# Performance work log

Hardware: AMD Instinct MI355X
Metric: run time of the kernel (lower is better)

The kernel has to match this reference:

```python
import jax, jax.numpy as jnp
import numpy as np
import math


def setup_inputs() -> dict:
    key = jax.random.key(0)
    ks = jax.random.split(key, 10)
    B, N, C, heads = 16, 1024, 256, 8
    nW = 4
    ANGLE_BINS = 5
    inner = C  # dim_head*heads == dim
    return {
        "x": jax.random.normal(ks[0], (B, N, C), jnp.float32),
        "mask": jax.random.normal(ks[1], (nW, N, N), jnp.float32),
        "affine_matrix": jax.random.normal(ks[2], (B, 2, 3), jnp.float32),
        "Wq": jax.random.normal(ks[3], (C, inner), jnp.float32) * (C ** -0.5),
        "bq": jnp.zeros((inner,), jnp.float32),
        "Wkv": jax.random.normal(ks[4], (C, 2 * inner), jnp.float32) * (C ** -0.5),
        "bkv": jnp.zeros((2 * inner,), jnp.float32),
        "Wp": jax.random.normal(ks[5], (C, C), jnp.float32) * (C ** -0.5),
        "bp": jnp.zeros((C,), jnp.float32),
        "angle_table": jnp.ones((ANGLE_BINS, heads), jnp.float32),
        "H": 32,
        "W": 32,
    }


def reference(x, mask, affine_matrix, Wq, bq, Wkv, bkv, Wp, bp, angle_table, H, W):
    B, N, C = x.shape
    heads = angle_table.shape[1]
    hd = C // heads
    scale = hd ** -0.5

    # qkv projections (torch Linear -> x @ W + b with W stored as (in, out))
    q = (x @ Wq + bq).reshape(B, N, heads, hd).transpose(0, 2, 1, 3)      # (B,h,N,d)
    kv = (x @ Wkv + bkv).reshape(B, N, 2, heads, hd).transpose(2, 0, 3, 1, 4)
    k, v = kv[0], kv[1]                                                    # (B,h,N,d)

    attn = jnp.einsum('bhqd,bhkd->bhqk', q * scale, k)                     # (B,h,N,N)

    # angle bias: per-query multiplicative bias in (1,2)
    grid_y, grid_x = jnp.meshgrid(jnp.arange(H), jnp.arange(W), indexing='ij')
    coords = jnp.stack([grid_x.reshape(-1), grid_y.reshape(-1)], -1).astype(jnp.float32)  # (N,2)
    center = jnp.array([W / 2.0, H / 2.0], jnp.float32)
    ego = jnp.einsum('bij,j->bi', affine_matrix[:, :2, :2], center) + affine_matrix[:, :2, 2]  # (B,2)
    rel = coords[None, :, :] - ego[:, None, :]                             # (B,N,2)
    ang = jnp.arctan2(rel[..., 1], rel[..., 0])
    bins = (((ang + math.pi) / (2.0 * math.pi)) * (angle_table.shape[0] - 1)).astype(jnp.int32)
    bias = 1.0 + jax.nn.sigmoid(angle_table[bins])                         # (B,N,h)
    attn = attn * bias.transpose(0, 2, 1)[..., None]                       # broadcast over keys

    # additive window mask then softmax
    nW = mask.shape[0]
    attn = attn.reshape(B // nW, nW, heads, N, N) + mask[None, :, None]
    attn = jax.nn.softmax(attn.reshape(B, heads, N, N), axis=-1)

    out = jnp.einsum('bhqk,bhkd->bhqd', attn, v).transpose(0, 2, 1, 3).reshape(B, N, C)
    return out @ Wp + bp
```

## Files before the change

kernel.cpp:

```cpp
#include <hip/hip_runtime.h>
#include <hip/hip_bf16.h>
#include <math.h>

#define BB 16
#define NTOK 1024
#define CDIM 256
#define HEADS 8
#define HD 32
#define LOG2E 1.4426950408889634f
#define PSHIFT 18.0f

typedef __attribute__((ext_vector_type(8))) _Float16 half8;
typedef __attribute__((ext_vector_type(4))) _Float16 half4v;
typedef __attribute__((ext_vector_type(8))) unsigned short u16x8;
typedef __attribute__((ext_vector_type(4))) unsigned int u32x4;
typedef __attribute__((ext_vector_type(4))) float f32x4;

__device__ __forceinline__ unsigned short f2h(float f) {
  _Float16 h = (_Float16)f;
  return __builtin_bit_cast(unsigned short, h);
}
__device__ __forceinline__ half8 ldh8(const unsigned short* p) {
  return *reinterpret_cast<const half8*>(p);
}
__device__ __forceinline__ void gl_lds16(const void* g, void* l) {
  __builtin_amdgcn_global_load_lds(
      (const __attribute__((address_space(1))) unsigned int*)g,
      (__attribute__((address_space(3))) unsigned int*)l, 16, 0, 0);
}

__global__ __launch_bounds__(256) void prep_xwb(
    const float* __restrict__ X, const float* __restrict__ Wq,
    const float* __restrict__ Wkv, const float* __restrict__ Wp,
    const float* __restrict__ affine, const float* __restrict__ atab,
    unsigned short* __restrict__ x16, unsigned short* __restrict__ wt16,
    unsigned short* __restrict__ wp16, float* __restrict__ bias) {
  int bid = blockIdx.x;
  if (bid < 2048) {
    size_t base = ((size_t)bid * 256 + threadIdx.x) * 8;
    float4 a = *(const float4*)(X + base);
    float4 b = *(const float4*)(X + base + 4);
    u16x8 o = {f2h(a.x), f2h(a.y), f2h(a.z), f2h(a.w),
               f2h(b.x), f2h(b.y), f2h(b.z), f2h(b.w)};
    *(u16x8*)(x16 + base) = o;
  } else if (bid < 3072) {
    int idx = (bid - 2048) * 256 + threadIdx.x;
    float val; size_t dst; bool isp = false;
    if (idx < 65536) {
      int k = idx >> 8, n = idx & 255;
      val = Wq[idx]; dst = (size_t)n * 256 + k;
    } else if (idx < 196608) {
      int i2 = idx - 65536;
      int k = i2 >> 9, n2 = i2 & 511;
      val = Wkv[i2]; dst = (size_t)(256 + n2) * 256 + k;
    } else {
      int i3 = idx - 196608;
      int k = i3 >> 8, n = i3 & 255;
      val = Wp[i3]; dst = (size_t)n * 256 + k; isp = true;
    }
    unsigned short h = f2h(val);
    if (isp) wp16[dst] = h; else wt16[dst] = h;
  } else {
    int idx = (bid - 3072) * 256 + threadIdx.x;
    if (idx >= BB * NTOK) return;
    int b = idx >> 10, n = idx & (NTOK - 1);
    float cx = (float)(n & 31);
    float cy = (float)(n >> 5);
    const float* A = affine + b * 6;
    float egx = fmaf(A[0], 16.f, fmaf(A[1], 16.f, A[2]));
    float egy = fmaf(A[3], 16.f, fmaf(A[4], 16.f, A[5]));
    float ang = atan2f(cy - egy, cx - egx);
    float t = (ang + 3.14159265358979323846f) *
              (1.f / (2.f * 3.14159265358979323846f)) * 4.f;
    int bin = (int)t;
    bin = bin < 0 ? 0 : (bin > 4 ? 4 : bin);
    for (int h = 0; h < HEADS; ++h) {
      float a = atab[bin * HEADS + h];
      float s = 1.f / (1.f + __expf(-a));
      bias[((size_t)b * HEADS + h) * NTOK + n] = 1.f + s;
    }
  }
}

__global__ __launch_bounds__(512, 4) void gemm_qkv16(
    const unsigned short* __restrict__ x16, const unsigned short* __restrict__ wt16,
    const float* __restrict__ bq, const float* __restrict__ bkv,
    const float* __restrict__ bias, const float* __restrict__ mask,
    unsigned short* __restrict__ q16, unsigned short* __restrict__ k16,
    unsigned short* __restrict__ vt16, unsigned short* __restrict__ mF16) {
  __shared__ __align__(16) unsigned short SM[16384];
  int bid = blockIdx.x;
  if (bid >= 768) {
    int idx = (bid - 768) * 512 + threadIdx.x;
    int b4 = idx >> 18;
    int rem = idx & 262143;
    int q = rem >> 8;
    int k = (rem & 255) * 4;
    float4 v = *(const float4*)(mask + ((size_t)b4 * NTOK + q) * NTOK + k);
    int kt = k >> 5;
    int ins0 = (k & 31) >> 1;
    int gw = (ins0 >> 2) ^ ((q >> 2) & 3);
    int io = ins0 & 3;
    size_t off = (size_t)q * 16 + gw * 4 + io;
    size_t slabE = ((size_t)(b4 * 64 + kt * 2)) * 16384;
    unsigned eP = (unsigned)f2h(v.x * LOG2E) |
                  ((unsigned)f2h(v.z * LOG2E) << 16);
    unsigned oP = (unsigned)f2h(v.y * LOG2E) |
                  ((unsigned)f2h(v.w * LOG2E) << 16);
    *(unsigned*)(mF16 + slabE + off) = eP;
    *(unsigned*)(mF16 + slabE + 16384 + off) = oP;
    return;
  }
  unsigned short* Xs = SM;
  unsigned short* Ws = SM + 8192;
  int tid = threadIdx.x;
  int w = tid >> 6, l = tid & 63;
  int row16 = l & 15, grp = l >> 4;
  int xcd = bid & 7, local = bid >> 3;
  int jb = local % 6, mb = xcd * 16 + local / 6;
  int j0 = jb * 128, m0 = mb * 128;
  int wm = w >> 1, wn = w & 1;

  auto stg = [&](int nb, int kt) {
    int k0s = kt * 32;
    int row = w * 16 + (l >> 2);
    int ge = (((l & 3) * 16) ^ ((row & 3) << 4)) >> 1;
    gl_lds16(x16 + (size_t)(m0 + row) * 256 + k0s + ge, Xs + nb * 4096 + w * 512);
    gl_lds16(wt16 + (size_t)(j0 + row) * 256 + k0s + ge, Ws + nb * 4096 + w * 512);
  };
  auto off16 = [&](int row, int g) {
    return row * 32 + ((((g * 16) ^ ((row & 3) << 4))) >> 1);
  };

  stg(0, 0);
  __syncthreads();

  f32x4 acc[2][4];
#pragma unroll
  for (int i = 0; i < 2; ++i)
#pragma unroll
    for (int c = 0; c < 4; ++c) acc[i][c] = (f32x4){0.f, 0.f, 0.f, 0.f};

  for (int kt = 0; kt < 8; ++kt) {
    int cur = kt & 1;
    if (kt < 7) stg(cur ^ 1, kt + 1);
    half8 a0 = ldh8(Xs + cur * 4096 + off16(wm * 32 + row16, grp));
    half8 a1 = ldh8(Xs + cur * 4096 + off16(wm * 32 + 16 + row16, grp));
#pragma unroll
    for (int c = 0; c < 4; ++c) {
      half8 bh = ldh8(Ws + cur * 4096 + off16(wn * 64 + c * 16 + row16, grp));
      acc[0][c] = __builtin_amdgcn_mfma_f32_16x16x32_f16(a0, bh, acc[0][c], 0, 0, 0);
      acc[1][c] = __builtin_amdgcn_mfma_f32_16x16x32_f16(a1, bh, acc[1][c], 0, 0, 0);
    }
    __syncthreads();
  }

  const float scaleq = 0.17677669529663687f * LOG2E;
  int half_mine = wm >> 1;
  for (int half = 0; half < 2; ++half) {
    if (half_mine == half) {
#pragma unroll
      for (int i = 0; i < 2; ++i) {
#pragma unroll
        for (int c = 0; c < 4; ++c) {
          int col = wn * 64 + c * 16 + row16;
          int jg = j0 + col;
#pragma unroll
          for (int r = 0; r < 4; ++r) {
            int rowl = (wm & 1) * 32 + i * 16 + grp * 4 + r;
            int m = m0 + half * 64 + rowl;
            int b = m >> 10, n = m & (NTOK - 1);
            float val = acc[i][c][r];
            unsigned short o;
            if (jb < 2)
              o = f2h((val + bq[jg]) * scaleq *
                      bias[((size_t)b * HEADS + (jg >> 5)) * NTOK + n]);
            else
              o = f2h(val + bkv[jg - CDIM]);
            SM[rowl * 136 + col] = o;
          }
        }
      }
    }
    __syncthreads();
    if (jb < 4) {
#pragma unroll
      for (int it = 0; it < 2; ++it) {
        int lin = it * 512 + tid;
        int rowb = lin >> 4, oct = lin & 15;
        u16x8 v = *(const u16x8*)&SM[rowb * 136 + oct * 8];
        int m = m0 + half * 64 + rowb;
        int b = m >> 10, n = m & (NTOK - 1);
        int jg = j0 + oct * 8;
        unsigned short* dst; int h, d;
        if (jb < 2) { h = jg >> 5; d = jg & 31; dst = q16; }
        else { int c2 = jg - CDIM; h = c2 >> 5; d = c2 & 31; dst = k16; }
        *(u16x8*)(dst + (((size_t)b * HEADS + h) * NTOK + n) * HD + d) = v;
      }
    } else {
#pragma unroll
      for (int it = 0; it < 2; ++it) {
        int lin = it * 512 + tid;
        int noct = lin >> 7, jl = lin & 127;
        u16x8 v;
#pragma unroll
        for (int e = 0; e < 8; ++e) v[e] = SM[(noct * 8 + e) * 136 + jl];
        int c3 = j0 + jl - 2 * CDIM;
        int h = c3 >> 5, d = c3 & 31;
        int n0 = m0 + half * 64 + noct * 8;
        int b = n0 >> 10, nn = n0 & (NTOK - 1);
        *(u16x8*)(vt16 + (((size_t)b * HEADS + h) * HD + d) * NTOK + nn) = v;
      }
    }
    __syncthreads();
  }
}

__global__ __launch_bounds__(512, 4) void attn16(
    const unsigned short* __restrict__ q16, const unsigned short* __restrict__ k16,
    const unsigned short* __restrict__ vt16, const unsigned short* __restrict__ mF16,
    unsigned short* __restrict__ ao16) {
  __shared__ __align__(16) unsigned short KT[2][4][1024];
  __shared__ __align__(16) unsigned short VT[2][4][1024];
  __shared__ __align__(16) unsigned short MT[2][2][1024];

  int tid = threadIdx.x;
  int w = tid >> 6, l = tid & 63;
  int row16 = l & 15, grp = l >> 4;
  int bid = blockIdx.x;
  int g = (bid >> 6) * 8 + (bid & 7);
  int inner = (bid >> 3) & 7;
  int qt = g >> 2, b4 = g & 3;
  int brep = inner >> 1, hg = inner & 1;
  int b = brep * 4 + b4;
  int hl = w >> 1, qh = w & 1;
  int head = hg * 4 + hl;
  int bh = b * HEADS + head;
  int q0g = qt * 64;
  int qbase = q0g + qh * 32;

  half8 bq[2];
#pragma unroll
  for (int qb = 0; qb < 2; ++qb)
    bq[qb] = ldh8(q16 + ((size_t)bh * NTOK + qbase + qb * 16 + row16) * HD +
                  grp * 8);

  const unsigned short* mFb = mF16 + (size_t)b4 * 64 * 16384;

  f32x4 acc[2][2];
#pragma unroll
  for (int i = 0; i < 2; ++i)
#pragma unroll
    for (int j = 0; j < 2; ++j) acc[i][j] = (f32x4){0.f, 0.f, 0.f, 0.f};
  float lsum[2] = {0.f, 0.f};
  const f32x4 c18 = (f32x4){-PSHIFT, -PSHIFT, -PSHIFT, -PSHIFT};

  auto off32 = [&](int row, int gg) {
    return row * 32 + ((gg ^ ((row >> 1) & 3)) << 3);
  };

  auto stage = [&](int nb, int kt2) {
    int k0n = (kt2 & 31) * 32;
    int key = 2 * (l >> 2) + qh;
    int sk = (l & 3) ^ ((qh * 8 + (l >> 3)) & 3);
    gl_lds16(k16 + ((size_t)bh * NTOK + k0n + key) * HD + sk * 8,
             &KT[nb][hl][qh * 512]);
    int dl = qh * 16 + (l >> 2);
    int sv = (l & 3) ^ ((qh * 8 + (l >> 3)) & 3);
    gl_lds16(vt16 + ((size_t)bh * HD + dl) * NTOK + k0n + sv * 8,
             &VT[nb][hl][qh * 512]);
    if (w < 4) {
      int slab = w >> 1, ch = w & 1;
      gl_lds16(mFb + (size_t)((kt2 & 31) * 2 + slab) * 16384 + q0g * 16 +
                   ch * 512 + l * 8,
               &MT[nb][slab][ch * 512]);
    }
  };

  stage(0, 0);
  __syncthreads();

  for (int kt = 0; kt < 32; ++kt) {
    int cur = kt & 1;
    if (kt < 31) stage(cur ^ 1, kt + 1);

    half8 kf0 = ldh8(&KT[cur][hl][off32(row16, grp)]);
    half8 kf1 = ldh8(&KT[cur][hl][off32(16 + row16, grp)]);
    half8 v0 = ldh8(&VT[cur][hl][off32(row16, grp)]);
    half8 v1 = ldh8(&VT[cur][hl][off32(16 + row16, grp)]);

#pragma unroll
    for (int qb = 0; qb < 2; ++qb) {
      int qr = qh * 32 + qb * 16 + row16;
      int g2 = grp ^ ((qr >> 2) & 3);
      half4v me = *(const half4v*)&MT[cur][0][qr * 16 + g2 * 4];
      half4v mo = *(const half4v*)&MT[cur][1][qr * 16 + g2 * 4];
      f32x4 s0 = __builtin_amdgcn_mfma_f32_16x16x32_f16(kf0, bq[qb], c18, 0, 0, 0);
      f32x4 s1 = __builtin_amdgcn_mfma_f32_16x16x32_f16(kf1, bq[qb], c18, 0, 0, 0);
      f32x4 e0, e1;
#pragma unroll
      for (int r = 0; r < 4; ++r) {
        e0[r] = __builtin_amdgcn_exp2f(s0[r] + (float)me[r]);
        e1[r] = __builtin_amdgcn_exp2f(s1[r] + (float)mo[r]);
      }
      lsum[qb] += ((e0[0] + e1[0]) + (e0[1] + e1[1])) +
                  ((e0[2] + e1[2]) + (e0[3] + e1[3]));
      u32x4 pk;
#pragma unroll
      for (int r = 0; r < 4; ++r)
        pk[r] = __builtin_bit_cast(unsigned,
                                   __builtin_amdgcn_cvt_pkrtz(e0[r], e1[r]));
      half8 pa = __builtin_bit_cast(half8, pk);
      acc[qb][0] = __builtin_amdgcn_mfma_f32_16x16x32_f16(pa, v0, acc[qb][0], 0, 0, 0);
      acc[qb][1] = __builtin_amdgcn_mfma_f32_16x16x32_f16(pa, v1, acc[qb][1], 0, 0, 0);
    }
    __syncthreads();
  }

#pragma unroll
  for (int qb = 0; qb < 2; ++qb) {
    lsum[qb] += __shfl_xor(lsum[qb], 16);
    lsum[qb] += __shfl_xor(lsum[qb], 32);
  }
#pragma unroll
  for (int qb = 0; qb < 2; ++qb) {
#pragma unroll
    for (int r = 0; r < 4; ++r) {
      float lr = __shfl(lsum[qb], grp * 4 + r, 16);
      float inv = 1.f / lr;
      int qrow = qbase + qb * 16 + grp * 4 + r;
      size_t obase = ((size_t)b * NTOK + qrow) * CDIM + head * HD;
      ao16[obase + row16] = f2h(acc[qb][0][r] * inv);
      ao16[obase + 16 + row16] = f2h(acc[qb][1][r] * inv);
    }
  }
}

__global__ __launch_bounds__(512, 4) void gemm_out16(
    const unsigned short* __restrict__ a16, const unsigned short* __restrict__ wp16,
    const float* __restrict__ bp, float* __restrict__ out) {
  __shared__ __align__(16) unsigned short SM[16384];
  unsigned short* Xs = SM;
  unsigned short* Ws = SM + 8192;
  int tid = threadIdx.x;
  int w = tid >> 6, l = tid & 63;
  int row16 = l & 15, grp = l >> 4;
  int bid = blockIdx.x;
  int xcd = bid & 7, local = bid >> 3;
  int jb = local & 1, mb = xcd * 16 + (local >> 1);
  int j0 = jb * 128, m0 = mb * 128;
  int wm = w >> 1, wn = w & 1;

  auto stg = [&](int nb, int kt) {
    int k0s = kt * 32;
    int row = w * 16 + (l >> 2);
    int ge = (((l & 3) * 16) ^ ((row & 3) << 4)) >> 1;
    gl_lds16(a16 + (size_t)(m0 + row) * 256 + k0s + ge, Xs + nb * 4096 + w * 512);
    gl_lds16(wp16 + (size_t)(j0 + row) * 256 + k0s + ge, Ws + nb * 4096 + w * 512);
  };
  auto off16 = [&](int row, int g) {
    return row * 32 + ((((g * 16) ^ ((row & 3) << 4))) >> 1);
  };

  stg(0, 0);
  __syncthreads();

  f32x4 acc[2][4];
#pragma unroll
  for (int i = 0; i < 2; ++i)
#pragma unroll
    for (int c = 0; c < 4; ++c) acc[i][c] = (f32x4){0.f, 0.f, 0.f, 0.f};

  for (int kt = 0; kt < 8; ++kt) {
    int cur = kt & 1;
    if (kt < 7) stg(cur ^ 1, kt + 1);
    half8 a0 = ldh8(Xs + cur * 4096 + off16(wm * 32 + row16, grp));
    half8 a1 = ldh8(Xs + cur * 4096 + off16(wm * 32 + 16 + row16, grp));
#pragma unroll
    for (int c = 0; c < 4; ++c) {
      half8 bh = ldh8(Ws + cur * 4096 + off16(wn * 64 + c * 16 + row16, grp));
      acc[0][c] = __builtin_amdgcn_mfma_f32_16x16x32_f16(a0, bh, acc[0][c], 0, 0, 0);
      acc[1][c] = __builtin_amdgcn_mfma_f32_16x16x32_f16(a1, bh, acc[1][c], 0, 0, 0);
    }
    __syncthreads();
  }

#pragma unroll
  for (int i = 0; i < 2; ++i) {
    int ng = m0 + wm * 32 + i * 16 + grp * 4;
#pragma unroll
    for (int c = 0; c < 4; ++c) {
      int jg = j0 + wn * 64 + c * 16 + row16;
      float bias = bp[jg];
#pragma unroll
      for (int r = 0; r < 4; ++r) {
        out[(size_t)(ng + r) * CDIM + jg] = acc[i][c][r] + bias;
      }
    }
  }
}

extern "C" void kernel_launch(void* const* d_in, const int* in_sizes, int n_in,
                              void* d_out, int out_size, void* d_ws,
                              size_t ws_size, hipStream_t stream) {
  const float* x = (const float*)d_in[0];
  const float* mask = (const float*)d_in[1];
  const float* affine = (const float*)d_in[2];
  const float* Wq = (const float*)d_in[3];
  const float* bq = (const float*)d_in[4];
  const float* Wkv = (const float*)d_in[5];
  const float* bkv = (const float*)d_in[6];
  const float* Wp = (const float*)d_in[7];
  const float* bp = (const float*)d_in[8];
  const float* atab = (const float*)d_in[9];
  float* out = (float*)d_out;

  const size_t bhnd = (size_t)BB * HEADS * NTOK * HD;
  unsigned short* q16 = (unsigned short*)d_ws;
  unsigned short* k16 = q16 + bhnd;
  unsigned short* vt16 = k16 + bhnd;
  unsigned short* x16 = vt16 + bhnd;
  unsigned short* wt16 = x16 + bhnd;
  unsigned short* wp16 = wt16 + 768 * 256;
  unsigned short* mF16 = wp16 + 256 * 256;
  float* bias = (float*)(mF16 + (size_t)4 * 64 * 16384);

  prep_xwb<<<3136, 256, 0, stream>>>(x, Wq, Wkv, Wp, affine, atab, x16, wt16,
                                     wp16, bias);
  gemm_qkv16<<<2816, 512, 0, stream>>>(x16, wt16, bq, bkv, bias, mask, q16,
                                       k16, vt16, mF16);
  attn16<<<512, 512, 0, stream>>>(q16, k16, vt16, mF16, x16);
  gemm_out16<<<256, 512, 0, stream>>>(x16, wp16, bp, out);
}
```

Measured before the change: 85.70 us.

## Split attention blocks to two heads with 16 query rows per wave

Each attention block now covers 2 heads instead of 4, and each wave handles 16 query rows instead of 32. The grid doubles to 1024 blocks, launch bounds allow 8 blocks per SM, and the K/V/mask staging is spread across wave roles. The aim is more parallelism and occupancy, with less shared memory and fewer registers per block. The trade-off is that each K/V tile and mask tile is reused by fewer query rows, so more redundant loads go through L2.

```diff
diff --git a/kernel.cpp b/kernel.cpp
--- a/kernel.cpp
+++ b/kernel.cpp
@@ -216,43 +216,37 @@
   }
 }
 
-__global__ __launch_bounds__(512, 4) void attn16(
+__global__ __launch_bounds__(512, 8) void attn16(
     const unsigned short* __restrict__ q16, const unsigned short* __restrict__ k16,
     const unsigned short* __restrict__ vt16, const unsigned short* __restrict__ mF16,
     unsigned short* __restrict__ ao16) {
-  __shared__ __align__(16) unsigned short KT[2][4][1024];
-  __shared__ __align__(16) unsigned short VT[2][4][1024];
+  __shared__ __align__(16) unsigned short KT[2][2][1024];
+  __shared__ __align__(16) unsigned short VT[2][2][1024];
   __shared__ __align__(16) unsigned short MT[2][2][1024];
 
   int tid = threadIdx.x;
   int w = tid >> 6, l = tid & 63;
   int row16 = l & 15, grp = l >> 4;
   int bid = blockIdx.x;
-  int g = (bid >> 6) * 8 + (bid & 7);
-  int inner = (bid >> 3) & 7;
+  int g = (bid >> 7) * 8 + (bid & 7);
+  int inner = (bid >> 3) & 15;
   int qt = g >> 2, b4 = g & 3;
-  int brep = inner >> 1, hg = inner & 1;
+  int brep = inner >> 2, hg = inner & 3;
   int b = brep * 4 + b4;
-  int hl = w >> 1, qh = w & 1;
-  int head = hg * 4 + hl;
+  int hl = w & 1, role = w >> 1;
+  int head = hg * 2 + hl;
   int bh = b * HEADS + head;
   int q0g = qt * 64;
-  int qbase = q0g + qh * 32;
-
-  half8 bq[2];
-#pragma unroll
-  for (int qb = 0; qb < 2; ++qb)
-    bq[qb] = ldh8(q16 + ((size_t)bh * NTOK + qbase + qb * 16 + row16) * HD +
-                  grp * 8);
+
+  half8 bq16 = ldh8(q16 + ((size_t)bh * NTOK + q0g + role * 16 + row16) * HD +
+                    grp * 8);
 
   const unsigned short* mFb = mF16 + (size_t)b4 * 64 * 16384;
 
-  f32x4 acc[2][2];
-#pragma unroll
-  for (int i = 0; i < 2; ++i)
-#pragma unroll
-    for (int j = 0; j < 2; ++j) acc[i][j] = (f32x4){0.f, 0.f, 0.f, 0.f};
-  float lsum[2] = {0.f, 0.f};
+  f32x4 acc[2];
+  acc[0] = (f32x4){0.f, 0.f, 0.f, 0.f};
+  acc[1] = (f32x4){0.f, 0.f, 0.f, 0.f};
+  float lsum = 0.f;
   const f32x4 c18 = (f32x4){-PSHIFT, -PSHIFT, -PSHIFT, -PSHIFT};
 
   auto off32 = [&](int row, int gg) {
@@ -261,16 +255,22 @@
 
   auto stage = [&](int nb, int kt2) {
     int k0n = (kt2 & 31) * 32;
-    int key = 2 * (l >> 2) + qh;
-    int sk = (l & 3) ^ ((qh * 8 + (l >> 3)) & 3);
-    gl_lds16(k16 + ((size_t)bh * NTOK + k0n + key) * HD + sk * 8,
-             &KT[nb][hl][qh * 512]);
-    int dl = qh * 16 + (l >> 2);
-    int sv = (l & 3) ^ ((qh * 8 + (l >> 3)) & 3);
-    gl_lds16(vt16 + ((size_t)bh * HD + dl) * NTOK + k0n + sv * 8,
-             &VT[nb][hl][qh * 512]);
-    if (w < 4) {
-      int slab = w >> 1, ch = w & 1;
+    if (role < 2) {
+      int c = role;
+      int r = c * 16 + (l >> 2);
+      int key = 2 * (l >> 2) + c;
+      int sk = (l & 3) ^ ((r >> 1) & 3);
+      gl_lds16(k16 + ((size_t)bh * NTOK + k0n + key) * HD + sk * 8,
+               &KT[nb][hl][c * 512]);
+    } else {
+      int c = role - 2;
+      int dl = c * 16 + (l >> 2);
+      int sv = (l & 3) ^ ((dl >> 1) & 3);
+      gl_lds16(vt16 + ((size_t)bh * HD + dl) * NTOK + k0n + sv * 8,
+               &VT[nb][hl][c * 512]);
+    }
+    if (hl == 0) {
+      int slab = role >> 1, ch = role & 1;
       gl_lds16(mFb + (size_t)((kt2 & 31) * 2 + slab) * 16384 + q0g * 16 +
                    ch * 512 + l * 8,
                &MT[nb][slab][ch * 512]);
@@ -289,50 +289,41 @@
     half8 v0 = ldh8(&VT[cur][hl][off32(row16, grp)]);
     half8 v1 = ldh8(&VT[cur][hl][off32(16 + row16, grp)]);
 
-#pragma unroll
-    for (int qb = 0; qb < 2; ++qb) {
-      int qr = qh * 32 + qb * 16 + row16;
-      int g2 = grp ^ ((qr >> 2) & 3);
-      half4v me = *(const half4v*)&MT[cur][0][qr * 16 + g2 * 4];
-      half4v mo = *(const half4v*)&MT[cur][1][qr * 16 + g2 * 4];
-      f32x4 s0 = __builtin_amdgcn_mfma_f32_16x16x32_f16(kf0, bq[qb], c18, 0, 0, 0);
-      f32x4 s1 = __builtin_amdgcn_mfma_f32_16x16x32_f16(kf1, bq[qb], c18, 0, 0, 0);
-      f32x4 e0, e1;
-#pragma unroll
-      for (int r = 0; r < 4; ++r) {
-        e0[r] = __builtin_amdgcn_exp2f(s0[r] + (float)me[r]);
-        e1[r] = __builtin_amdgcn_exp2f(s1[r] + (float)mo[r]);
-      }
-      lsum[qb] += ((e0[0] + e1[0]) + (e0[1] + e1[1])) +
-                  ((e0[2] + e1[2]) + (e0[3] + e1[3]));
-      u32x4 pk;
-#pragma unroll
-      for (int r = 0; r < 4; ++r)
-        pk[r] = __builtin_bit_cast(unsigned,
-                                   __builtin_amdgcn_cvt_pkrtz(e0[r], e1[r]));
-      half8 pa = __builtin_bit_cast(half8, pk);
-      acc[qb][0] = __builtin_amdgcn_mfma_f32_16x16x32_f16(pa, v0, acc[qb][0], 0, 0, 0);
-      acc[qb][1] = __builtin_amdgcn_mfma_f32_16x16x32_f16(pa, v1, acc[qb][1], 0, 0, 0);
-    }
+    int qr = role * 16 + row16;
+    int g2 = grp ^ ((qr >> 2) & 3);
+    half4v me = *(const half4v*)&MT[cur][0][qr * 16 + g2 * 4];
+    half4v mo = *(const half4v*)&MT[cur][1][qr * 16 + g2 * 4];
+    f32x4 s0 = __builtin_amdgcn_mfma_f32_16x16x32_f16(kf0, bq16, c18, 0, 0, 0);
+    f32x4 s1 = __builtin_amdgcn_mfma_f32_16x16x32_f16(kf1, bq16, c18, 0, 0, 0);
+    f32x4 e0, e1;
+#pragma unroll
+    for (int r = 0; r < 4; ++r) {
+      e0[r] = __builtin_amdgcn_exp2f(s0[r] + (float)me[r]);
+      e1[r] = __builtin_amdgcn_exp2f(s1[r] + (float)mo[r]);
+    }
+    lsum += ((e0[0] + e1[0]) + (e0[1] + e1[1])) +
+            ((e0[2] + e1[2]) + (e0[3] + e1[3]));
+    u32x4 pk;
+#pragma unroll
+    for (int r = 0; r < 4; ++r)
+      pk[r] = __builtin_bit_cast(unsigned,
+                                 __builtin_amdgcn_cvt_pkrtz(e0[r], e1[r]));
+    half8 pa = __builtin_bit_cast(half8, pk);
+    acc[0] = __builtin_amdgcn_mfma_f32_16x16x32_f16(pa, v0, acc[0], 0, 0, 0);
+    acc[1] = __builtin_amdgcn_mfma_f32_16x16x32_f16(pa, v1, acc[1], 0, 0, 0);
     __syncthreads();
   }
 
-#pragma unroll
-  for (int qb = 0; qb < 2; ++qb) {
-    lsum[qb] += __shfl_xor(lsum[qb], 16);
-    lsum[qb] += __shfl_xor(lsum[qb], 32);
-  }
-#pragma unroll
-  for (int qb = 0; qb < 2; ++qb) {
-#pragma unroll
-    for (int r = 0; r < 4; ++r) {
-      float lr = __shfl(lsum[qb], grp * 4 + r, 16);
-      float inv = 1.f / lr;
-      int qrow = qbase + qb * 16 + grp * 4 + r;
-      size_t obase = ((size_t)b * NTOK + qrow) * CDIM + head * HD;
-      ao16[obase + row16] = f2h(acc[qb][0][r] * inv);
-      ao16[obase + 16 + row16] = f2h(acc[qb][1][r] * inv);
-    }
+  lsum += __shfl_xor(lsum, 16);
+  lsum += __shfl_xor(lsum, 32);
+#pragma unroll
+  for (int r = 0; r < 4; ++r) {
+    float lr = __shfl(lsum, grp * 4 + r, 16);
+    float inv = 1.f / lr;
+    int qrow = q0g + role * 16 + grp * 4 + r;
+    size_t obase = ((size_t)b * NTOK + qrow) * CDIM + head * HD;
+    ao16[obase + row16] = f2h(acc[0][r] * inv);
+    ao16[obase + 16 + row16] = f2h(acc[1][r] * inv);
   }
 }
 
@@ -429,6 +420,6 @@
                                      wp16, bias);
   gemm_qkv16<<<2816, 512, 0, stream>>>(x16, wt16, bq, bkv, bias, mask, q16,
                                        k16, vt16, mF16);
-  attn16<<<512, 512, 0, stream>>>(q16, k16, vt16, mF16, x16);
+  attn16<<<1024, 512, 0, stream>>>(q16, k16, vt16, mF16, x16);
   gemm_out16<<<256, 512, 0, stream>>>(x16, wp16, bp, out);
 }
```

After: 85.77 us. No clear change (+0.1%).
